# Optimization experiments

Hardware: AMD Instinct MI355X
Metric: run time of the kernel (lower is better)

The kernel has to match this reference:

```python
import jax, jax.numpy as jnp
import numpy as np

D_MODEL = 1024
N_HEAD = 16
D_HEAD = D_MODEL // N_HEAD
NEG = -1e9


def setup_inputs() -> dict:
    key = jax.random.key(0)
    ks = jax.random.split(key, 11)
    B, T, C = 4, 2048, D_MODEL
    s = 1.0 / np.sqrt(C)
    return {
        "q": jax.random.normal(ks[0], (B, T, C), jnp.float32),
        "k": jax.random.normal(ks[1], (B, T, C), jnp.float32),
        "v": jax.random.normal(ks[2], (B, T, C), jnp.float32),
        "w_q": jax.random.normal(ks[3], (C, C), jnp.float32) * s,
        "b_q": jnp.zeros((C,), jnp.float32),
        "w_k": jax.random.normal(ks[4], (C, C), jnp.float32) * s,
        "b_k": jnp.zeros((C,), jnp.float32),
        "w_v": jax.random.normal(ks[5], (C, C), jnp.float32) * s,
        "b_v": jnp.zeros((C,), jnp.float32),
        "w_o": jax.random.normal(ks[6], (C, C), jnp.float32) * s,
        "b_o": jnp.zeros((C,), jnp.float32),
    }


def reference(q, k, v, w_q, b_q, w_k, b_k, w_v, b_v, w_o, b_o):
    B, T, C = q.shape
    # projections; weights stored as [in, out]
    qh = (q @ w_q + b_q).reshape(B, T, N_HEAD, D_HEAD).transpose(0, 2, 1, 3)
    kh = (k @ w_k + b_k).reshape(B, T, N_HEAD, D_HEAD).transpose(0, 2, 1, 3)
    vh = (v @ w_v + b_v).reshape(B, T, N_HEAD, D_HEAD).transpose(0, 2, 1, 3)
    scores = jnp.einsum("bhqd,bhkd->bhqk", qh, kh) / jnp.sqrt(
        jnp.asarray(D_HEAD, qh.dtype))
    causal = jnp.tril(jnp.ones((T, T), dtype=bool))  # [T,T]
    scores = jnp.where(causal[None, None], scores, NEG)
    attn = jax.nn.softmax(scores, axis=-1)
    out = jnp.einsum("bhqk,bhkd->bhqd", attn, vh)
    out = out.transpose(0, 2, 1, 3).reshape(B, T, C)
    return out @ w_o + b_o
```

## Files before the change

kernel.cpp:

```cpp
#include <hip/hip_runtime.h>
#include <hip/hip_bf16.h>
#include <cstdint>
#include <cstddef>

#define DEVI static __device__ __forceinline__

typedef __attribute__((ext_vector_type(8))) short short8;
typedef __attribute__((ext_vector_type(4))) float f32x4;

typedef __attribute__((address_space(1))) const unsigned int as1c_uint;
typedef __attribute__((address_space(3))) unsigned int as3_uint;

constexpr int Bn = 4, Tn = 2048, Cn = 1024, Hn = 16, Dn = 64;
constexpr int Mtot = Bn * Tn;
#define QSCALE (0.125f * 1.44269504088896340736f)

DEVI unsigned short f2bf(float f) {
  unsigned u = __float_as_uint(f);
  u += 0x7fffu + ((u >> 16) & 1u);
  return (unsigned short)(u >> 16);
}
DEVI unsigned short f2bf_t(float f) {
  return (unsigned short)(__float_as_uint(f) >> 16);
}

DEVI void async16(const void* g, void* l) {
  __builtin_amdgcn_global_load_lds((as1c_uint*)g, (as3_uint*)l, 16, 0, 0);
}

__global__ __launch_bounds__(256) void cvt3_kernel(
    const float4* __restrict__ i0, const float4* __restrict__ i1,
    const float4* __restrict__ i2, ushort4* __restrict__ o0,
    ushort4* __restrict__ o1, ushort4* __restrict__ o2, int n4, int zoff) {
  const int z = blockIdx.y + zoff;
  const float4* in = z == 0 ? i0 : z == 1 ? i1 : i2;
  ushort4* out = z == 0 ? o0 : z == 1 ? o1 : o2;
  const int stride = gridDim.x * blockDim.x;
  for (int i = blockIdx.x * blockDim.x + threadIdx.x; i < n4; i += stride) {
    float4 v = in[i];
    ushort4 o;
    o.x = f2bf(v.x); o.y = f2bf(v.y); o.z = f2bf(v.z); o.w = f2bf(v.w);
    out[i] = o;
  }
}

__global__ __launch_bounds__(256) void transpose_cvt4(
    const float* __restrict__ w0, const float* __restrict__ w1,
    const float* __restrict__ w2, const float* __restrict__ w3,
    unsigned short* __restrict__ o0, unsigned short* __restrict__ o1,
    unsigned short* __restrict__ o2, unsigned short* __restrict__ o3) {
  __shared__ float tile[32][33];
  const int z = blockIdx.z;
  const float* w = z == 0 ? w0 : z == 1 ? w1 : z == 2 ? w2 : w3;
  unsigned short* wT = z == 0 ? o0 : z == 1 ? o1 : z == 2 ? o2 : o3;
  int n0 = blockIdx.x * 32, k0 = blockIdx.y * 32;
  int tx = threadIdx.x, ty = threadIdx.y;
#pragma unroll
  for (int r = 0; r < 32; r += 8)
    tile[ty + r][tx] = w[(size_t)(k0 + ty + r) * Cn + n0 + tx];
  __syncthreads();
#pragma unroll
  for (int r = 0; r < 32; r += 8)
    wT[(size_t)(n0 + ty + r) * Cn + k0 + tx] = f2bf(tile[tx][ty + r]);
}

DEVI void stage256(const unsigned short* __restrict__ g, int ld, int m0, int k0,
                   unsigned short* lds, int w, int lane) {
#pragma unroll
  for (int j = 0; j < 4; ++j) {
    int s = j * 512 + w * 64 + lane;
    int row = s >> 3;
    int col = ((s & 7) ^ (row & 7)) * 8;
    async16(g + (size_t)(m0 + row) * ld + k0 + col,
            lds + (size_t)(j * 512 + w * 64) * 8);
  }
}

DEVI void gemm8p_core(const unsigned short* __restrict__ A,
                      const unsigned short* __restrict__ BT, int K,
                      int m0, int n0, int tid, f32x4 (&acc)[8][4]) {
  __shared__ unsigned short As[2][256 * 64];
  __shared__ unsigned short Bs[2][256 * 64];
  const int lane = tid & 63, w = tid >> 6;
  const int wm = w >> 2, wn = w & 3;
  const int l15 = lane & 15, l4 = lane >> 4;
  const int NT = K >> 6;

  stage256(A, K, m0, 0, As[0], w, lane);
  stage256(BT, K, n0, 0, Bs[0], w, lane);
  stage256(A, K, m0, 64, As[1], w, lane);
  stage256(BT, K, n0, 64, Bs[1], w, lane);

  const int arow = wm * 128 + l15;
  const int brow = wn * 64 + l15;

#pragma unroll 1
  for (int kt = 0; kt < NT; ++kt) {
    const int c = kt & 1;
    if (kt + 1 < NT) {
      asm volatile("s_waitcnt vmcnt(8)" ::: "memory");
    } else {
      asm volatile("s_waitcnt vmcnt(0)" ::: "memory");
    }
    __builtin_amdgcn_s_barrier();
    __builtin_amdgcn_sched_barrier(0);
    const unsigned short* Ab = As[c];
    const unsigned short* Bb = Bs[c];

    short8 bfr[4][2];
#pragma unroll
    for (int j = 0; j < 4; ++j)
#pragma unroll
      for (int kk = 0; kk < 2; ++kk) {
        int r = brow + j * 16;
        bfr[j][kk] = *(const short8*)&Bb[r * 64 + (((kk * 4 + l4) ^ (r & 7)) * 8)];
      }

#pragma unroll
    for (int ph = 0; ph < 4; ++ph) {
      short8 af[2][2];
#pragma unroll
      for (int ii = 0; ii < 2; ++ii)
#pragma unroll
        for (int kk = 0; kk < 2; ++kk) {
          int r = arow + (ph * 2 + ii) * 16;
          af[ii][kk] = *(const short8*)&Ab[r * 64 + (((kk * 4 + l4) ^ (r & 7)) * 8)];
        }
      if (ph == 3) {
        asm volatile("s_waitcnt lgkmcnt(0)" ::: "memory");
        __builtin_amdgcn_s_barrier();
        __builtin_amdgcn_sched_barrier(0);
        if (kt + 2 < NT) {
          stage256(A, K, m0, (kt + 2) * 64, As[c], w, lane);
          stage256(BT, K, n0, (kt + 2) * 64, Bs[c], w, lane);
        }
      }
      __builtin_amdgcn_s_setprio(1);
#pragma unroll
      for (int ii = 0; ii < 2; ++ii)
#pragma unroll
        for (int j = 0; j < 4; ++j)
#pragma unroll
          for (int kk = 0; kk < 2; ++kk)
            acc[ph * 2 + ii][j] = __builtin_amdgcn_mfma_f32_16x16x32_bf16(
                af[ii][kk], bfr[j][kk], acc[ph * 2 + ii][j], 0, 0, 0);
      __builtin_amdgcn_s_setprio(0);
    }
  }
}

__global__ __launch_bounds__(512, 2) void gemm8p_qkv(
    const unsigned short* __restrict__ Aq, const unsigned short* __restrict__ Ak,
    const unsigned short* __restrict__ Av, const unsigned short* __restrict__ Bq,
    const unsigned short* __restrict__ Bk, const unsigned short* __restrict__ Bv,
    const float* __restrict__ bq, const float* __restrict__ bk,
    const float* __restrict__ bv, unsigned short* __restrict__ oq,
    unsigned short* __restrict__ ok, unsigned short* __restrict__ ov, int zoff) {
  const int z = blockIdx.z + zoff;
  const unsigned short* A = z == 0 ? Aq : z == 1 ? Ak : Av;
  const unsigned short* BT = z == 0 ? Bq : z == 1 ? Bk : Bv;
  const float* bias = z == 0 ? bq : z == 1 ? bk : bv;
  unsigned short* o = z == 0 ? oq : z == 1 ? ok : ov;

  const int tid = threadIdx.x;
  const int lane = tid & 63, w = tid >> 6;
  const int wm = w >> 2, wn = w & 3;
  const int l15 = lane & 15, l4 = lane >> 4;
  const int fid = blockIdx.y * 32 + blockIdx.x;
  const int swz = (fid & 7) * 16 + (fid >> 3);
  const int m0 = (swz & 31) * 256, n0 = (swz >> 5) * 256;

  const f32x4 zf = {0.f, 0.f, 0.f, 0.f};
  f32x4 acc[8][4];
#pragma unroll
  for (int i = 0; i < 8; ++i)
#pragma unroll
    for (int j = 0; j < 4; ++j) acc[i][j] = zf;

  gemm8p_core(A, BT, Cn, m0, n0, tid, acc);

#pragma unroll
  for (int j = 0; j < 4; ++j) {
    int n = n0 + wn * 64 + j * 16 + l15;
    float bvl = bias[n];
    int h = n >> 6, d = n & 63;
#pragma unroll
    for (int i = 0; i < 8; ++i) {
      int mbase = m0 + wm * 128 + i * 16 + l4 * 4;
      if (z < 2) {
        float scale = z == 0 ? QSCALE : 1.f;
#pragma unroll
        for (int r = 0; r < 4; ++r) {
          int m = mbase + r;
          int b = m >> 11, t = m & 2047;
          o[((size_t)((b * Hn + h) * Tn + t)) * Dn + d] = f2bf((acc[i][j][r] + bvl) * scale);
        }
      } else {
        int b = mbase >> 11, t0 = mbase & 2047;
        ushort4 pk;
        pk.x = f2bf(acc[i][j][0] + bvl);
        pk.y = f2bf(acc[i][j][1] + bvl);
        pk.z = f2bf(acc[i][j][2] + bvl);
        pk.w = f2bf(acc[i][j][3] + bvl);
        *(ushort4*)&o[((size_t)((b * Hn + h) * Dn + d)) * Tn + t0] = pk;
      }
    }
  }
}

__global__ __launch_bounds__(512, 2) void gemm8p_out(
    const unsigned short* __restrict__ A, const unsigned short* __restrict__ BT,
    const float* __restrict__ bias, float* __restrict__ o) {
  const int tid = threadIdx.x;
  const int lane = tid & 63, w = tid >> 6;
  const int wm = w >> 2, wn = w & 3;
  const int l15 = lane & 15, l4 = lane >> 4;
  const int fid = blockIdx.y * 32 + blockIdx.x;
  const int swz = (fid & 7) * 16 + (fid >> 3);
  const int m0 = (swz & 31) * 256, n0 = (swz >> 5) * 256;

  const f32x4 zf = {0.f, 0.f, 0.f, 0.f};
  f32x4 acc[8][4];
#pragma unroll
  for (int i = 0; i < 8; ++i)
#pragma unroll
    for (int j = 0; j < 4; ++j) acc[i][j] = zf;

  gemm8p_core(A, BT, Cn, m0, n0, tid, acc);

#pragma unroll
  for (int j = 0; j < 4; ++j) {
    int n = n0 + wn * 64 + j * 16 + l15;
    float bvl = bias[n];
#pragma unroll
    for (int i = 0; i < 8; ++i) {
      int mbase = m0 + wm * 128 + i * 16 + l4 * 4;
#pragma unroll
      for (int r = 0; r < 4; ++r)
        o[(size_t)(mbase + r) * Cn + n] = acc[i][j][r] + bvl;
    }
  }
}

__global__ __launch_bounds__(512) void attn_kernel(const unsigned short* __restrict__ qh,
                                                   const unsigned short* __restrict__ kh,
                                                   const unsigned short* __restrict__ vt,
                                                   unsigned short* __restrict__ obf) {
  __shared__ unsigned short Ks[2][64 * 64];
  __shared__ unsigned short Vs[2][64 * 64];
  __shared__ unsigned short Ps[8][16 * 72];

  const int tid = threadIdx.x, lane = tid & 63, w = tid >> 6;
  const int l15 = lane & 15, l4 = lane >> 4;
  const int swz = l15 & 7;

  const int bid = blockIdx.x;
  const int j = bid >> 3;
  const int bh = (bid & 7) * 8 + (j & 7);
  const int pair = j >> 3;
  const unsigned short* qb = qh + (size_t)bh * Tn * Dn;
  const unsigned short* kb = kh + (size_t)bh * Tn * Dn;
  const unsigned short* vb = vt + (size_t)bh * Dn * Tn;
  const int b = bh >> 4, h = bh & 15;

  const int srow = lane >> 3, sslot = (lane & 7) ^ (lane >> 3);

  const f32x4 z = {0.f, 0.f, 0.f, 0.f};
  const short ob = (short)0x3F80;
  const short8 ones = {ob, ob, ob, ob, ob, ob, ob, ob};

#pragma unroll 1
  for (int half = 0; half < 2; ++half) {
    const int qt = half == 0 ? pair : 15 - pair;
    const int q0 = qt * 128;
    const int qrow = q0 + w * 16 + l15;

    short8 qf0 = *(const short8*)(qb + (size_t)qrow * Dn + l4 * 8);
    short8 qf1 = *(const short8*)(qb + (size_t)qrow * Dn + 32 + l4 * 8);

    f32x4 o[4];
#pragma unroll
    for (int nd = 0; nd < 4; ++nd) o[nd] = z;
    f32x4 osum = z;

    const int nt = (q0 >> 6) + 2;
    const int ntw = ((q0 + w * 16 + 15) >> 6) + 1;

    {
      const unsigned short* ksrc = kb + (size_t)(w * 8 + srow) * Dn + sslot * 8;
      const unsigned short* vsrc = vb + (size_t)(w * 8 + srow) * Tn + sslot * 8;
      async16(ksrc, &Ks[0][w * 512]);
      async16(vsrc, &Vs[0][w * 512]);
    }

#pragma unroll 1
    for (int t = 0; t < nt; ++t) {
      const int cur = t & 1;
      if (t + 1 < nt) {
        const int kv1 = (t + 1) * 64;
        const unsigned short* ksrc = kb + (size_t)(kv1 + w * 8 + srow) * Dn + sslot * 8;
        const unsigned short* vsrc = vb + (size_t)(w * 8 + srow) * Tn + kv1 + sslot * 8;
        async16(ksrc, &Ks[cur ^ 1][w * 512]);
        async16(vsrc, &Vs[cur ^ 1][w * 512]);
        asm volatile("s_waitcnt vmcnt(2)" ::: "memory");
      } else {
        asm volatile("s_waitcnt vmcnt(0)" ::: "memory");
      }
      __builtin_amdgcn_s_barrier();
      __builtin_amdgcn_sched_barrier(0);

      if (t < ntw) {
        const unsigned short* Kc = &Ks[cur][0];
        const unsigned short* Vc = &Vs[cur][0];

        f32x4 s[4];
#pragma unroll
        for (int ni = 0; ni < 4; ++ni) s[ni] = z;
        __builtin_amdgcn_s_setprio(1);
#pragma unroll
        for (int ni = 0; ni < 4; ++ni) {
          const int rb = (ni * 16 + l15) * 64;
          short8 kf0 = *(const short8*)&Kc[rb + ((l4 ^ swz) * 8)];
          short8 kf1 = *(const short8*)&Kc[rb + (((4 + l4) ^ swz) * 8)];
          s[ni] = __builtin_amdgcn_mfma_f32_16x16x32_bf16(kf0, qf0, s[ni], 0, 0, 0);
          s[ni] = __builtin_amdgcn_mfma_f32_16x16x32_bf16(kf1, qf1, s[ni], 0, 0, 0);
        }
        __builtin_amdgcn_s_setprio(0);

        short8 vf[8];
#pragma unroll
        for (int nd = 0; nd < 4; ++nd) {
          const int rb = (nd * 16 + l15) * 64;
          vf[nd * 2]     = *(const short8*)&Vc[rb + ((l4 ^ swz) * 8)];
          vf[nd * 2 + 1] = *(const short8*)&Vc[rb + (((4 + l4) ^ swz) * 8)];
        }

        const int kq = qrow - t * 64;
        const bool edge = (t * 64 + 63 > q0 + w * 16);
        if (!edge) {
#pragma unroll
          for (int ni = 0; ni < 4; ++ni) {
            ushort4 pk;
#pragma unroll
            for (int r = 0; r < 4; ++r)
              ((unsigned short*)&pk)[r] = f2bf_t(__builtin_amdgcn_exp2f(s[ni][r]));
            *(ushort4*)&Ps[w][l15 * 72 + ni * 16 + l4 * 4] = pk;
          }
        } else {
#pragma unroll
          for (int ni = 0; ni < 4; ++ni) {
            ushort4 pk;
#pragma unroll
            for (int r = 0; r < 4; ++r) {
              float e = __builtin_amdgcn_exp2f(s[ni][r]);
              if ((ni * 16 + l4 * 4 + r) > kq) e = 0.f;
              ((unsigned short*)&pk)[r] = f2bf_t(e);
            }
            *(ushort4*)&Ps[w][l15 * 72 + ni * 16 + l4 * 4] = pk;
          }
        }
        asm volatile("s_waitcnt lgkmcnt(0)" ::: "memory");
        __builtin_amdgcn_sched_barrier(0);

        short8 pf0 = *(const short8*)&Ps[w][l15 * 72 + l4 * 8];
        short8 pf1 = *(const short8*)&Ps[w][l15 * 72 + 32 + l4 * 8];
        __builtin_amdgcn_s_setprio(1);
        osum = __builtin_amdgcn_mfma_f32_16x16x32_bf16(pf0, ones, osum, 0, 0, 0);
        osum = __builtin_amdgcn_mfma_f32_16x16x32_bf16(pf1, ones, osum, 0, 0, 0);
#pragma unroll
        for (int nd = 0; nd < 4; ++nd) {
          o[nd] = __builtin_amdgcn_mfma_f32_16x16x32_bf16(pf0, vf[nd * 2], o[nd], 0, 0, 0);
          o[nd] = __builtin_amdgcn_mfma_f32_16x16x32_bf16(pf1, vf[nd * 2 + 1], o[nd], 0, 0, 0);
        }
        __builtin_amdgcn_s_setprio(0);
      }

      __builtin_amdgcn_sched_barrier(0);
      __builtin_amdgcn_s_barrier();
    }

#pragma unroll
    for (int r = 0; r < 4; ++r) {
      float inv = __builtin_amdgcn_rcpf(osum[r]);
      int tq = q0 + w * 16 + l4 * 4 + r;
      size_t base = ((size_t)(b * Tn + tq)) * Cn + h * 64;
#pragma unroll
      for (int nd = 0; nd < 4; ++nd)
        obf[base + nd * 16 + l15] = f2bf(o[nd][r] * inv);
    }
  }
}

extern "C" void kernel_launch(void* const* d_in, const int* in_sizes, int n_in,
                              void* d_out, int out_size, void* d_ws, size_t ws_size,
                              hipStream_t stream) {
  const float* q   = (const float*)d_in[0];
  const float* k   = (const float*)d_in[1];
  const float* v   = (const float*)d_in[2];
  const float* w_q = (const float*)d_in[3];
  const float* b_q = (const float*)d_in[4];
  const float* w_k = (const float*)d_in[5];
  const float* b_k = (const float*)d_in[6];
  const float* w_v = (const float*)d_in[7];
  const float* b_v = (const float*)d_in[8];
  const float* w_o = (const float*)d_in[9];
  const float* b_o = (const float*)d_in[10];

  char* ws = (char*)d_ws;
  const size_t MB = 1u << 20;
  const bool big = ws_size >= 104 * MB;
  const int n4 = Mtot * Cn / 4;
  dim3 gg(Mtot / 256, Cn / 256, 1);

  unsigned short *xq, *xk, *xv, *qhp, *khp, *vtp, *wqT, *wkT, *wvT, *woT;
  if (big) {
    xq  = (unsigned short*)(ws);
    xk  = (unsigned short*)(ws + 16 * MB);
    xv  = (unsigned short*)(ws + 32 * MB);
    qhp = (unsigned short*)(ws + 48 * MB);
    khp = (unsigned short*)(ws + 64 * MB);
    vtp = (unsigned short*)(ws + 80 * MB);
    wqT = (unsigned short*)(ws + 96 * MB);
    wkT = (unsigned short*)(ws + 98 * MB);
    wvT = (unsigned short*)(ws + 100 * MB);
    woT = (unsigned short*)(ws + 102 * MB);
  } else {
    xq = xk = xv = (unsigned short*)(ws);
    wqT = (unsigned short*)(ws + 16 * MB);
    wkT = (unsigned short*)(ws + 18 * MB);
    wvT = (unsigned short*)(ws + 20 * MB);
    woT = (unsigned short*)(ws + 22 * MB);
    qhp = (unsigned short*)(ws + 24 * MB);
    khp = (unsigned short*)(ws + 40 * MB);
    vtp = (unsigned short*)(ws + 56 * MB);
  }
  unsigned short* aout = xq;

  transpose_cvt4<<<dim3(32, 32, 4), dim3(32, 8), 0, stream>>>(
      w_q, w_k, w_v, w_o, wqT, wkT, wvT, woT);

  if (big) {
    cvt3_kernel<<<dim3(2048, 3), 256, 0, stream>>>(
        (const float4*)q, (const float4*)k, (const float4*)v,
        (ushort4*)xq, (ushort4*)xk, (ushort4*)xv, n4, 0);
    dim3 g3(Mtot / 256, Cn / 256, 3);
    gemm8p_qkv<<<g3, 512, 0, stream>>>(xq, xk, xv, wqT, wkT, wvT,
                                       b_q, b_k, b_v, qhp, khp, vtp, 0);
  } else {
    for (int z = 0; z < 3; ++z) {
      cvt3_kernel<<<dim3(2048, 1), 256, 0, stream>>>(
          (const float4*)q, (const float4*)k, (const float4*)v,
          (ushort4*)xq, (ushort4*)xq, (ushort4*)xq, n4, z);
      gemm8p_qkv<<<gg, 512, 0, stream>>>(xq, xq, xq, wqT, wkT, wvT,
                                         b_q, b_k, b_v, qhp, khp, vtp, z);
    }
  }

  attn_kernel<<<512, 512, 0, stream>>>(qhp, khp, vtp, aout);

  gemm8p_out<<<gg, 512, 0, stream>>>(aout, woT, b_o, (float*)d_out);
}
```

Before: 195.6 us.

## Shrink GEMM tiles to 256x128 and flatten QKV grid to fill all CUs

Changes the projection GEMM block tile from 256x256 to 256x128, so each of the 8 waves computes a 64x64 sub-tile instead of 128x64. This doubles the block count per GEMM (256 instead of 128) so that more compute units have work. The QKV launch becomes a 1D grid of 768 blocks that indexes Q/K/V from contiguous workspace buffers, and the L2-friendly block swizzle is dropped. In exchange, each block reuses loaded A data less and the GEMMs move more data from L2 in total, and the flattened indexing relies on xq/xk/xv sitting contiguously in the big-workspace layout.

```diff
diff --git a/kernel.cpp b/kernel.cpp
--- a/kernel.cpp
+++ b/kernel.cpp
@@ -64,41 +64,39 @@
     wT[(size_t)(n0 + ty + r) * Cn + k0 + tx] = f2bf(tile[tx][ty + r]);
 }
 
-DEVI void stage256(const unsigned short* __restrict__ g, int ld, int m0, int k0,
-                   unsigned short* lds, int w, int lane) {
-#pragma unroll
-  for (int j = 0; j < 4; ++j) {
+template <int R>
+DEVI void stageR(const unsigned short* __restrict__ g, int ld, int r0, int k0,
+                 unsigned short* lds, int w, int lane) {
+#pragma unroll
+  for (int j = 0; j < R / 64; ++j) {
     int s = j * 512 + w * 64 + lane;
     int row = s >> 3;
     int col = ((s & 7) ^ (row & 7)) * 8;
-    async16(g + (size_t)(m0 + row) * ld + k0 + col,
+    async16(g + (size_t)(r0 + row) * ld + k0 + col,
             lds + (size_t)(j * 512 + w * 64) * 8);
   }
 }
 
 DEVI void gemm8p_core(const unsigned short* __restrict__ A,
                       const unsigned short* __restrict__ BT, int K,
-                      int m0, int n0, int tid, f32x4 (&acc)[8][4]) {
+                      int m0, int n0, int tid, f32x4 (&acc)[4][4]) {
   __shared__ unsigned short As[2][256 * 64];
-  __shared__ unsigned short Bs[2][256 * 64];
+  __shared__ unsigned short Bs[2][128 * 64];
   const int lane = tid & 63, w = tid >> 6;
-  const int wm = w >> 2, wn = w & 3;
+  const int wm = w >> 1, wn = w & 1;
   const int l15 = lane & 15, l4 = lane >> 4;
   const int NT = K >> 6;
 
-  stage256(A, K, m0, 0, As[0], w, lane);
-  stage256(BT, K, n0, 0, Bs[0], w, lane);
-  stage256(A, K, m0, 64, As[1], w, lane);
-  stage256(BT, K, n0, 64, Bs[1], w, lane);
-
-  const int arow = wm * 128 + l15;
-  const int brow = wn * 64 + l15;
+  stageR<256>(A, K, m0, 0, As[0], w, lane);
+  stageR<128>(BT, K, n0, 0, Bs[0], w, lane);
+  stageR<256>(A, K, m0, 64, As[1], w, lane);
+  stageR<128>(BT, K, n0, 64, Bs[1], w, lane);
 
 #pragma unroll 1
   for (int kt = 0; kt < NT; ++kt) {
     const int c = kt & 1;
     if (kt + 1 < NT) {
-      asm volatile("s_waitcnt vmcnt(8)" ::: "memory");
+      asm volatile("s_waitcnt vmcnt(6)" ::: "memory");
     } else {
       asm volatile("s_waitcnt vmcnt(0)" ::: "memory");
     }
@@ -112,97 +110,89 @@
     for (int j = 0; j < 4; ++j)
 #pragma unroll
       for (int kk = 0; kk < 2; ++kk) {
-        int r = brow + j * 16;
+        int r = wn * 64 + j * 16 + l15;
         bfr[j][kk] = *(const short8*)&Bb[r * 64 + (((kk * 4 + l4) ^ (r & 7)) * 8)];
       }
 
 #pragma unroll
     for (int ph = 0; ph < 4; ++ph) {
-      short8 af[2][2];
-#pragma unroll
-      for (int ii = 0; ii < 2; ++ii)
-#pragma unroll
-        for (int kk = 0; kk < 2; ++kk) {
-          int r = arow + (ph * 2 + ii) * 16;
-          af[ii][kk] = *(const short8*)&Ab[r * 64 + (((kk * 4 + l4) ^ (r & 7)) * 8)];
-        }
+      short8 af[2];
+      {
+        int r = wm * 64 + ph * 16 + l15;
+        af[0] = *(const short8*)&Ab[r * 64 + ((l4 ^ (r & 7)) * 8)];
+        af[1] = *(const short8*)&Ab[r * 64 + (((4 + l4) ^ (r & 7)) * 8)];
+      }
       if (ph == 3) {
         asm volatile("s_waitcnt lgkmcnt(0)" ::: "memory");
         __builtin_amdgcn_s_barrier();
         __builtin_amdgcn_sched_barrier(0);
         if (kt + 2 < NT) {
-          stage256(A, K, m0, (kt + 2) * 64, As[c], w, lane);
-          stage256(BT, K, n0, (kt + 2) * 64, Bs[c], w, lane);
+          stageR<256>(A, K, m0, (kt + 2) * 64, As[c], w, lane);
+          stageR<128>(BT, K, n0, (kt + 2) * 64, Bs[c], w, lane);
         }
       }
       __builtin_amdgcn_s_setprio(1);
 #pragma unroll
-      for (int ii = 0; ii < 2; ++ii)
-#pragma unroll
-        for (int j = 0; j < 4; ++j)
-#pragma unroll
-          for (int kk = 0; kk < 2; ++kk)
-            acc[ph * 2 + ii][j] = __builtin_amdgcn_mfma_f32_16x16x32_bf16(
-                af[ii][kk], bfr[j][kk], acc[ph * 2 + ii][j], 0, 0, 0);
+      for (int j = 0; j < 4; ++j) {
+        acc[ph][j] = __builtin_amdgcn_mfma_f32_16x16x32_bf16(af[0], bfr[j][0], acc[ph][j], 0, 0, 0);
+        acc[ph][j] = __builtin_amdgcn_mfma_f32_16x16x32_bf16(af[1], bfr[j][1], acc[ph][j], 0, 0, 0);
+      }
       __builtin_amdgcn_s_setprio(0);
     }
   }
 }
 
 __global__ __launch_bounds__(512, 2) void gemm8p_qkv(
-    const unsigned short* __restrict__ Aq, const unsigned short* __restrict__ Ak,
-    const unsigned short* __restrict__ Av, const unsigned short* __restrict__ Bq,
-    const unsigned short* __restrict__ Bk, const unsigned short* __restrict__ Bv,
-    const float* __restrict__ bq, const float* __restrict__ bk,
-    const float* __restrict__ bv, unsigned short* __restrict__ oq,
-    unsigned short* __restrict__ ok, unsigned short* __restrict__ ov, int zoff) {
-  const int z = blockIdx.z + zoff;
-  const unsigned short* A = z == 0 ? Aq : z == 1 ? Ak : Av;
+    const unsigned short* __restrict__ A,
+    const unsigned short* __restrict__ Bq, const unsigned short* __restrict__ Bk,
+    const unsigned short* __restrict__ Bv, const float* __restrict__ bq,
+    const float* __restrict__ bk, const float* __restrict__ bv,
+    unsigned short* __restrict__ oq, unsigned short* __restrict__ ok,
+    unsigned short* __restrict__ ov, int zoff) {
+  const int tid = threadIdx.x;
+  const int lane = tid & 63, w = tid >> 6;
+  const int wm = w >> 1, wn = w & 1;
+  const int l15 = lane & 15, l4 = lane >> 4;
+  const int fid = blockIdx.x;
+  const int nt = fid & 7, mt = fid >> 3;
+  const int m0 = mt * 256, n0 = nt * 128;
+  const int z = zoff + (mt >> 5);
+
   const unsigned short* BT = z == 0 ? Bq : z == 1 ? Bk : Bv;
   const float* bias = z == 0 ? bq : z == 1 ? bk : bv;
-  unsigned short* o = z == 0 ? oq : z == 1 ? ok : ov;
-
-  const int tid = threadIdx.x;
-  const int lane = tid & 63, w = tid >> 6;
-  const int wm = w >> 2, wn = w & 3;
-  const int l15 = lane & 15, l4 = lane >> 4;
-  const int fid = blockIdx.y * 32 + blockIdx.x;
-  const int swz = (fid & 7) * 16 + (fid >> 3);
-  const int m0 = (swz & 31) * 256, n0 = (swz >> 5) * 256;
 
   const f32x4 zf = {0.f, 0.f, 0.f, 0.f};
-  f32x4 acc[8][4];
-#pragma unroll
-  for (int i = 0; i < 8; ++i)
+  f32x4 acc[4][4];
+#pragma unroll
+  for (int i = 0; i < 4; ++i)
 #pragma unroll
     for (int j = 0; j < 4; ++j) acc[i][j] = zf;
 
   gemm8p_core(A, BT, Cn, m0, n0, tid, acc);
 
+  const int mloc = m0 & 8191;
 #pragma unroll
   for (int j = 0; j < 4; ++j) {
     int n = n0 + wn * 64 + j * 16 + l15;
     float bvl = bias[n];
     int h = n >> 6, d = n & 63;
 #pragma unroll
-    for (int i = 0; i < 8; ++i) {
-      int mbase = m0 + wm * 128 + i * 16 + l4 * 4;
+    for (int i = 0; i < 4; ++i) {
+      int mbase = mloc + wm * 64 + i * 16 + l4 * 4;
+      int b = mbase >> 11, t0 = mbase & 2047;
       if (z < 2) {
+        unsigned short* o = z == 0 ? oq : ok;
         float scale = z == 0 ? QSCALE : 1.f;
 #pragma unroll
-        for (int r = 0; r < 4; ++r) {
-          int m = mbase + r;
-          int b = m >> 11, t = m & 2047;
-          o[((size_t)((b * Hn + h) * Tn + t)) * Dn + d] = f2bf((acc[i][j][r] + bvl) * scale);
-        }
+        for (int r = 0; r < 4; ++r)
+          o[((size_t)((b * Hn + h) * Tn + t0 + r)) * Dn + d] = f2bf((acc[i][j][r] + bvl) * scale);
       } else {
-        int b = mbase >> 11, t0 = mbase & 2047;
         ushort4 pk;
         pk.x = f2bf(acc[i][j][0] + bvl);
         pk.y = f2bf(acc[i][j][1] + bvl);
         pk.z = f2bf(acc[i][j][2] + bvl);
         pk.w = f2bf(acc[i][j][3] + bvl);
-        *(ushort4*)&o[((size_t)((b * Hn + h) * Dn + d)) * Tn + t0] = pk;
+        *(ushort4*)&ov[((size_t)((b * Hn + h) * Dn + d)) * Tn + t0] = pk;
       }
     }
   }
@@ -213,16 +203,16 @@
     const float* __restrict__ bias, float* __restrict__ o) {
   const int tid = threadIdx.x;
   const int lane = tid & 63, w = tid >> 6;
-  const int wm = w >> 2, wn = w & 3;
+  const int wm = w >> 1, wn = w & 1;
   const int l15 = lane & 15, l4 = lane >> 4;
-  const int fid = blockIdx.y * 32 + blockIdx.x;
-  const int swz = (fid & 7) * 16 + (fid >> 3);
-  const int m0 = (swz & 31) * 256, n0 = (swz >> 5) * 256;
+  const int fid = blockIdx.x;
+  const int nt = fid & 7, mt = fid >> 3;
+  const int m0 = mt * 256, n0 = nt * 128;
 
   const f32x4 zf = {0.f, 0.f, 0.f, 0.f};
-  f32x4 acc[8][4];
-#pragma unroll
-  for (int i = 0; i < 8; ++i)
+  f32x4 acc[4][4];
+#pragma unroll
+  for (int i = 0; i < 4; ++i)
 #pragma unroll
     for (int j = 0; j < 4; ++j) acc[i][j] = zf;
 
@@ -233,8 +223,8 @@
     int n = n0 + wn * 64 + j * 16 + l15;
     float bvl = bias[n];
 #pragma unroll
-    for (int i = 0; i < 8; ++i) {
-      int mbase = m0 + wm * 128 + i * 16 + l4 * 4;
+    for (int i = 0; i < 4; ++i) {
+      int mbase = m0 + wm * 64 + i * 16 + l4 * 4;
 #pragma unroll
       for (int r = 0; r < 4; ++r)
         o[(size_t)(mbase + r) * Cn + n] = acc[i][j][r] + bvl;
@@ -410,7 +400,6 @@
   const size_t MB = 1u << 20;
   const bool big = ws_size >= 104 * MB;
   const int n4 = Mtot * Cn / 4;
-  dim3 gg(Mtot / 256, Cn / 256, 1);
 
   unsigned short *xq, *xk, *xv, *qhp, *khp, *vtp, *wqT, *wkT, *wvT, *woT;
   if (big) {
@@ -443,20 +432,19 @@
     cvt3_kernel<<<dim3(2048, 3), 256, 0, stream>>>(
         (const float4*)q, (const float4*)k, (const float4*)v,
         (ushort4*)xq, (ushort4*)xk, (ushort4*)xv, n4, 0);
-    dim3 g3(Mtot / 256, Cn / 256, 3);
-    gemm8p_qkv<<<g3, 512, 0, stream>>>(xq, xk, xv, wqT, wkT, wvT,
-                                       b_q, b_k, b_v, qhp, khp, vtp, 0);
+    gemm8p_qkv<<<768, 512, 0, stream>>>(xq, wqT, wkT, wvT,
+                                        b_q, b_k, b_v, qhp, khp, vtp, 0);
   } else {
     for (int z = 0; z < 3; ++z) {
       cvt3_kernel<<<dim3(2048, 1), 256, 0, stream>>>(
           (const float4*)q, (const float4*)k, (const float4*)v,
           (ushort4*)xq, (ushort4*)xq, (ushort4*)xq, n4, z);
-      gemm8p_qkv<<<gg, 512, 0, stream>>>(xq, xq, xq, wqT, wkT, wvT,
-                                         b_q, b_k, b_v, qhp, khp, vtp, z);
+      gemm8p_qkv<<<256, 512, 0, stream>>>(xq, wqT, wkT, wvT,
+                                          b_q, b_k, b_v, qhp, khp, vtp, z);
     }
   }
 
   attn_kernel<<<512, 512, 0, stream>>>(qhp, khp, vtp, aout);
 
-  gemm8p_out<<<gg, 512, 0, stream>>>(aout, woT, b_o, (float*)d_out);
-}
+  gemm8p_out<<<256, 512, 0, stream>>>(aout, woT, b_o, (float*)d_out);
+}
```

New measurement: 192.1 us. No clear change (-1.8%).
